# Kernel tuning notes

Hardware: AMD Instinct MI355X
Metric: run time of the kernel (lower is better)

## Reference

```python
import jax, jax.numpy as jnp
import numpy as np

N = 8192       # nodes
F_IN = 512     # input features
H = 8          # heads (layer 1)
C1 = 8         # per-head channels (layer 1)
NC = 16        # num classes
E = 262144     # edges (avg degree 32)
NEG_SLOPE = 0.2


def setup_inputs() -> dict:
    key = jax.random.key(0)
    ks = jax.random.split(key, 11)
    s = 0.1
    return {
        "x": jax.random.normal(ks[0], (N, F_IN), jnp.float32),
        "edge_index": jax.random.randint(ks[1], (2, E), 0, N, dtype=jnp.int32),
        "W1": jax.random.normal(ks[2], (F_IN, H * C1), jnp.float32) * s,
        "a_src1": jax.random.normal(ks[3], (H, C1), jnp.float32) * s,
        "a_dst1": jax.random.normal(ks[4], (H, C1), jnp.float32) * s,
        "b1": jnp.zeros((H * C1,), jnp.float32),
        "W2": jax.random.normal(ks[5], (H * C1, NC), jnp.float32) * s,
        "a_src2": jax.random.normal(ks[6], (1, NC), jnp.float32) * s,
        "a_dst2": jax.random.normal(ks[7], (1, NC), jnp.float32) * s,
        "b2": jnp.zeros((NC,), jnp.float32),
    }


def _gat_layer(x, W, a_src, a_dst, b, src, dst, heads, outc, concat):
    n = x.shape[0]
    h = (x @ W).reshape(n, heads, outc)                      # [N,H,C]
    al_s = jnp.einsum('nhc,hc->nh', h, a_src)                 # [N,H]
    al_d = jnp.einsum('nhc,hc->nh', h, a_dst)                 # [N,H]
    e = jax.nn.leaky_relu(al_s[src] + al_d[dst], NEG_SLOPE)   # [E,H]
    # segment softmax over destination node (every node has a self-loop)
    m = jax.ops.segment_max(e, dst, num_segments=n)
    ex = jnp.exp(e - m[dst])
    denom = jax.ops.segment_sum(ex, dst, num_segments=n)
    alpha = ex / denom[dst]                                   # [E,H]
    out = jax.ops.segment_sum(alpha[:, :, None] * h[src], dst, num_segments=n)  # [N,H,C]
    out = out.reshape(n, heads * outc) if concat else out.mean(axis=1)
    return out + b


def reference(x, edge_index, W1, a_src1, a_dst1, b1, W2, a_src2, a_dst2, b2):
    # add self-loops (PyG GATConv default)
    loop = jnp.arange(N, dtype=edge_index.dtype)
    src = jnp.concatenate([edge_index[0], loop])
    dst = jnp.concatenate([edge_index[1], loop])
    # dropout layers are identity in eval mode
    h1 = jax.nn.elu(_gat_layer(x, W1, a_src1, a_dst1, b1, src, dst, H, C1, True))
    z = _gat_layer(h1, W2, a_src2, a_dst2, b2, src, dst, 1, NC, False)
    return jax.nn.log_softmax(z, axis=-1), z @ z.T
```

## Files before the change

kernel.cpp:

```cpp
#include <hip/hip_runtime.h>
#include <math.h>

#define N_NODES 8192
#define F_IN 512
#define NH1 8
#define C1 8
#define D1 64
#define NC 16
#define E_EDGES 262144
#define TOT_EDGES (E_EDGES + N_NODES)
#define NEG_SLOPE 0.2f

__global__ __launch_bounds__(256) void gemm1_k(const float* __restrict__ x,
                                               const float* __restrict__ W1,
                                               float* __restrict__ h1pre) {
    __shared__ __align__(16) float As[32 * 68];
    __shared__ __align__(16) float Bs[32 * 68];
    int tid = threadIdx.x;
    int rowBase = blockIdx.x * 64;
    int rm = tid >> 4, rn = tid & 15;
    float acc[4][4] = {};
    for (int k0 = 0; k0 < F_IN; k0 += 32) {
#pragma unroll
        for (int j = 0; j < 8; ++j) {
            int i = tid + 256 * j;
            int r = i >> 5, c = i & 31;
            As[c * 68 + r] = x[(rowBase + r) * F_IN + k0 + c];
        }
#pragma unroll
        for (int j = 0; j < 8; ++j) {
            int i = tid + 256 * j;
            int rr = i >> 6, cc = i & 63;
            Bs[rr * 68 + cc] = W1[(k0 + rr) * D1 + cc];
        }
        __syncthreads();
#pragma unroll
        for (int kk = 0; kk < 32; ++kk) {
            float4 a = *(const float4*)&As[kk * 68 + rm * 4];
            float4 b = *(const float4*)&Bs[kk * 68 + rn * 4];
            float av[4] = {a.x, a.y, a.z, a.w};
            float bv[4] = {b.x, b.y, b.z, b.w};
#pragma unroll
            for (int jj = 0; jj < 4; ++jj)
#pragma unroll
                for (int ll = 0; ll < 4; ++ll)
                    acc[jj][ll] = fmaf(av[jj], bv[ll], acc[jj][ll]);
        }
        __syncthreads();
    }
#pragma unroll
    for (int jj = 0; jj < 4; ++jj) {
        float4 o = {acc[jj][0], acc[jj][1], acc[jj][2], acc[jj][3]};
        *(float4*)&h1pre[(size_t)(rowBase + rm * 4 + jj) * D1 + rn * 4] = o;
    }
}

__global__ void logits1_k(const float* __restrict__ h1pre,
                          const float* __restrict__ a_src1, const float* __restrict__ a_dst1,
                          float* __restrict__ als1, float* __restrict__ ald1) {
    int i = blockIdx.x * blockDim.x + threadIdx.x;
    if (i >= N_NODES * NH1) return;
    int h = i & 7;
    const float* hp = h1pre + (size_t)(i >> 3) * D1 + h * C1;
    float s = 0.f, d = 0.f;
#pragma unroll
    for (int c = 0; c < C1; ++c) {
        float v = hp[c];
        s = fmaf(v, a_src1[h * C1 + c], s);
        d = fmaf(v, a_dst1[h * C1 + c], d);
    }
    als1[i] = s;
    ald1[i] = d;
}

__global__ void hist_k(const int* __restrict__ ei, int* __restrict__ counts) {
    int i = blockIdx.x * blockDim.x + threadIdx.x;
    if (i >= TOT_EDGES) return;
    int dst = (i < E_EDGES) ? ei[E_EDGES + i] : (i - E_EDGES);
    atomicAdd(&counts[dst], 1);
}

__global__ __launch_bounds__(1024) void scan_k(const int* __restrict__ counts,
                                               int* __restrict__ offsets, int* __restrict__ cursor) {
    __shared__ int part[1024];
    int t = threadIdx.x;
    int local[8];
    int s = 0;
#pragma unroll
    for (int j = 0; j < 8; ++j) { local[j] = counts[t * 8 + j]; s += local[j]; }
    part[t] = s;
    __syncthreads();
    for (int d = 1; d < 1024; d <<= 1) {
        int v = (t >= d) ? part[t - d] : 0;
        __syncthreads();
        part[t] += v;
        __syncthreads();
    }
    int run = (t == 0) ? 0 : part[t - 1];
#pragma unroll
    for (int j = 0; j < 8; ++j) {
        offsets[t * 8 + j] = run;
        cursor[t * 8 + j] = run;
        run += local[j];
    }
    if (t == 1023) offsets[8192] = run;
}

__global__ void scatter_k(const int* __restrict__ ei, int* __restrict__ cursor, int* __restrict__ csr) {
    int i = blockIdx.x * blockDim.x + threadIdx.x;
    if (i >= TOT_EDGES) return;
    int src, dst;
    if (i < E_EDGES) { src = ei[i]; dst = ei[E_EDGES + i]; }
    else             { src = i - E_EDGES; dst = src; }
    int pos = atomicAdd(&cursor[dst], 1);
    csr[pos] = src;
}

__global__ __launch_bounds__(64) void agg1_k(const float* __restrict__ h1pre,
                                             const float* __restrict__ als1, const float* __restrict__ ald1,
                                             const int* __restrict__ offsets, const int* __restrict__ csr,
                                             const float* __restrict__ b1, float* __restrict__ out1) {
    int n = blockIdx.x, t = threadIdx.x;
    int beg = offsets[n], end = offsets[n + 1];
    int h = t & 7;
    float aldh = ald1[n * NH1 + h];
    float m = -3.4e38f;
    for (int i = beg + (t >> 3); i < end; i += 8) {
        int s = csr[i];
        float v = als1[s * NH1 + h] + aldh;
        v = v > 0.f ? v : NEG_SLOPE * v;
        m = fmaxf(m, v);
    }
    m = fmaxf(m, __shfl_xor(m, 8));
    m = fmaxf(m, __shfl_xor(m, 16));
    m = fmaxf(m, __shfl_xor(m, 32));
    float den = 0.f;
    for (int i = beg + (t >> 3); i < end; i += 8) {
        int s = csr[i];
        float v = als1[s * NH1 + h] + aldh;
        v = v > 0.f ? v : NEG_SLOPE * v;
        den += expf(v - m);
    }
    den += __shfl_xor(den, 8);
    den += __shfl_xor(den, 16);
    den += __shfl_xor(den, 32);
    int q = t >> 3;
    float mq = __shfl(m, q);
    float dq = __shfl(den, q);
    float aldq = ald1[n * NH1 + q];
    float acc = 0.f;
    for (int i = beg; i < end; ++i) {
        int s = csr[i];
        float v = als1[s * NH1 + q] + aldq;
        v = v > 0.f ? v : NEG_SLOPE * v;
        float w = expf(v - mq);
        acc = fmaf(w, h1pre[(size_t)s * D1 + t], acc);
    }
    float val = acc / dq + b1[t];
    out1[(size_t)n * D1 + t] = val > 0.f ? val : expm1f(val);
}

__global__ __launch_bounds__(256) void gemm2_k(const float* __restrict__ out1,
                                               const float* __restrict__ W2,
                                               float* __restrict__ h2pre) {
    __shared__ float w2s[D1 * NC];
    __shared__ float ot[16 * D1];
    int tid = threadIdx.x;
    int nb = blockIdx.x * 16;
#pragma unroll
    for (int j = 0; j < 4; ++j) {
        w2s[tid + 256 * j] = W2[tid + 256 * j];
        ot[tid + 256 * j] = out1[(size_t)nb * D1 + tid + 256 * j];
    }
    __syncthreads();
    int nl = tid >> 4, c = tid & 15;
    float acc = 0.f;
#pragma unroll
    for (int k = 0; k < D1; ++k) acc = fmaf(ot[nl * D1 + k], w2s[k * NC + c], acc);
    h2pre[(size_t)(nb + nl) * NC + c] = acc;
}

__global__ void logits2_k(const float* __restrict__ h2pre,
                          const float* __restrict__ a_src2, const float* __restrict__ a_dst2,
                          float* __restrict__ als2, float* __restrict__ ald2) {
    int n = blockIdx.x * blockDim.x + threadIdx.x;
    if (n >= N_NODES) return;
    const float* hp = h2pre + (size_t)n * NC;
    float s = 0.f, d = 0.f;
#pragma unroll
    for (int c = 0; c < NC; ++c) {
        float v = hp[c];
        s = fmaf(v, a_src2[c], s);
        d = fmaf(v, a_dst2[c], d);
    }
    als2[n] = s;
    ald2[n] = d;
}

__global__ __launch_bounds__(64) void agg2_k(const float* __restrict__ h2pre,
                                             const float* __restrict__ als2, const float* __restrict__ ald2,
                                             const int* __restrict__ offsets, const int* __restrict__ csr,
                                             const float* __restrict__ b2,
                                             float* __restrict__ z, float* __restrict__ out_ls) {
    int n = blockIdx.x, t = threadIdx.x;
    int beg = offsets[n], end = offsets[n + 1];
    float aldn = ald2[n];
    float m = -3.4e38f;
    for (int i = beg + t; i < end; i += 64) {
        float v = als2[csr[i]] + aldn;
        v = v > 0.f ? v : NEG_SLOPE * v;
        m = fmaxf(m, v);
    }
#pragma unroll
    for (int d = 1; d < 64; d <<= 1) m = fmaxf(m, __shfl_xor(m, d));
    float den = 0.f;
    for (int i = beg + t; i < end; i += 64) {
        float v = als2[csr[i]] + aldn;
        v = v > 0.f ? v : NEG_SLOPE * v;
        den += expf(v - m);
    }
#pragma unroll
    for (int d = 1; d < 64; d <<= 1) den += __shfl_xor(den, d);
    int eg = t >> 4, c = t & 15;
    float acc = 0.f;
    for (int i = beg + eg; i < end; i += 4) {
        int s = csr[i];
        float v = als2[s] + aldn;
        v = v > 0.f ? v : NEG_SLOPE * v;
        acc = fmaf(expf(v - m), h2pre[(size_t)s * NC + c], acc);
    }
    acc += __shfl_xor(acc, 16);
    acc += __shfl_xor(acc, 32);
    float zv = acc / den + b2[c];
    if (t < 16) z[(size_t)n * NC + t] = zv;
    float zm = zv;
#pragma unroll
    for (int d = 1; d < 16; d <<= 1) zm = fmaxf(zm, __shfl_xor(zm, d));
    float se = expf(zv - zm);
#pragma unroll
    for (int d = 1; d < 16; d <<= 1) se += __shfl_xor(se, d);
    if (t < 16) out_ls[(size_t)n * NC + t] = zv - (zm + logf(se));
}

__global__ __launch_bounds__(256) void gram_k(const float* __restrict__ z,
                                              float* __restrict__ out) {
    __shared__ __align__(16) float rz[64 * 16];
    int tid = threadIdx.x;
    int colBase = blockIdx.x * 256;
    int rowBase = blockIdx.y * 64;
    ((float4*)rz)[tid] = ((const float4*)z)[rowBase * 4 + tid];
    int j = colBase + tid;
    float c[16];
#pragma unroll
    for (int k4 = 0; k4 < 4; ++k4) {
        float4 v = ((const float4*)(z + (size_t)j * 16))[k4];
        c[k4 * 4 + 0] = v.x; c[k4 * 4 + 1] = v.y; c[k4 * 4 + 2] = v.z; c[k4 * 4 + 3] = v.w;
    }
    __syncthreads();
#pragma unroll 4
    for (int r = 0; r < 64; ++r) {
        const float* zr = &rz[r * 16];
        float acc = 0.f;
#pragma unroll
        for (int k = 0; k < 16; ++k) acc = fmaf(c[k], zr[k], acc);
        out[(size_t)(rowBase + r) * N_NODES + j] = acc;
    }
}

extern "C" void kernel_launch(void* const* d_in, const int* in_sizes, int n_in,
                              void* d_out, int out_size, void* d_ws, size_t ws_size,
                              hipStream_t stream) {
    (void)in_sizes; (void)n_in; (void)out_size; (void)ws_size;
    const float* x      = (const float*)d_in[0];
    const int*   ei     = (const int*)d_in[1];
    const float* W1     = (const float*)d_in[2];
    const float* a_src1 = (const float*)d_in[3];
    const float* a_dst1 = (const float*)d_in[4];
    const float* b1     = (const float*)d_in[5];
    const float* W2     = (const float*)d_in[6];
    const float* a_src2 = (const float*)d_in[7];
    const float* a_dst2 = (const float*)d_in[8];
    const float* b2     = (const float*)d_in[9];
    float* out = (float*)d_out;

    char* ws = (char*)d_ws;
    float* h1pre  = (float*)(ws + 0);
    float* out1   = (float*)(ws + 2097152);
    float* als1   = (float*)(ws + 4194304);
    float* ald1   = (float*)(ws + 4456448);
    float* h2pre  = (float*)(ws + 4718592);
    float* als2   = (float*)(ws + 5242880);
    float* ald2   = (float*)(ws + 5275648);
    float* zarr   = (float*)(ws + 5308416);
    int*   counts = (int*)  (ws + 5832704);
    int*   offsets= (int*)  (ws + 5865472);
    int*   cursor = (int*)  (ws + 5898496);
    int*   csr    = (int*)  (ws + 5931264);

    hipMemsetAsync(counts, 0, N_NODES * sizeof(int), stream);
    hist_k<<<(TOT_EDGES + 255) / 256, 256, 0, stream>>>(ei, counts);
    scan_k<<<1, 1024, 0, stream>>>(counts, offsets, cursor);
    scatter_k<<<(TOT_EDGES + 255) / 256, 256, 0, stream>>>(ei, cursor, csr);

    gemm1_k<<<N_NODES / 64, 256, 0, stream>>>(x, W1, h1pre);
    logits1_k<<<(N_NODES * NH1 + 255) / 256, 256, 0, stream>>>(h1pre, a_src1, a_dst1, als1, ald1);
    agg1_k<<<N_NODES, 64, 0, stream>>>(h1pre, als1, ald1, offsets, csr, b1, out1);

    gemm2_k<<<N_NODES / 16, 256, 0, stream>>>(out1, W2, h2pre);
    logits2_k<<<N_NODES / 256, 256, 0, stream>>>(h2pre, a_src2, a_dst2, als2, ald2);
    agg2_k<<<N_NODES, 64, 0, stream>>>(h2pre, als2, ald2, offsets, csr, b2, zarr, out);

    gram_k<<<dim3(N_NODES / 256, N_NODES / 64), 256, 0, stream>>>(zarr, out + (size_t)N_NODES * NC);
}
```

Baseline: 405.0 us.

## Fuse logits into GEMMs, cache edge weights in LDS, shuffle-based scan

Computes the layer-1 attention logits in the gemm1 epilogue, with the tile halved to 32 rows for more blocks. The layer-2 GEMM and logits move into the agg1 epilogue, which removes three kernel launches and the out1 round trip through memory. agg1 and agg2 now store source indices and exponentiated edge weights in shared memory for nodes with degree up to 128, so the leaky-relu and exp are not recomputed in each pass. Higher-degree nodes fall back to the old path. The scan is rewritten to use wavefront shuffles instead of a shared-memory Hillis-Steele loop with many barriers.

```diff
diff --git a/kernel.cpp b/kernel.cpp
--- a/kernel.cpp
+++ b/kernel.cpp
@@ -10,22 +10,27 @@
 #define E_EDGES 262144
 #define TOT_EDGES (E_EDGES + N_NODES)
 #define NEG_SLOPE 0.2f
+#define CAP 128
 
 __global__ __launch_bounds__(256) void gemm1_k(const float* __restrict__ x,
                                                const float* __restrict__ W1,
-                                               float* __restrict__ h1pre) {
-    __shared__ __align__(16) float As[32 * 68];
+                                               const float* __restrict__ a_src1,
+                                               const float* __restrict__ a_dst1,
+                                               float* __restrict__ h1pre,
+                                               float* __restrict__ als1,
+                                               float* __restrict__ ald1) {
+    __shared__ __align__(16) float As[32 * 34];
     __shared__ __align__(16) float Bs[32 * 68];
     int tid = threadIdx.x;
-    int rowBase = blockIdx.x * 64;
+    int rowBase = blockIdx.x * 32;
     int rm = tid >> 4, rn = tid & 15;
-    float acc[4][4] = {};
+    float acc[2][4] = {};
     for (int k0 = 0; k0 < F_IN; k0 += 32) {
 #pragma unroll
-        for (int j = 0; j < 8; ++j) {
+        for (int j = 0; j < 4; ++j) {
             int i = tid + 256 * j;
             int r = i >> 5, c = i & 31;
-            As[c * 68 + r] = x[(rowBase + r) * F_IN + k0 + c];
+            As[c * 34 + r] = x[(rowBase + r) * F_IN + k0 + c];
         }
 #pragma unroll
         for (int j = 0; j < 8; ++j) {
@@ -36,41 +41,37 @@
         __syncthreads();
 #pragma unroll
         for (int kk = 0; kk < 32; ++kk) {
-            float4 a = *(const float4*)&As[kk * 68 + rm * 4];
+            float2 a = *(const float2*)&As[kk * 34 + rm * 2];
             float4 b = *(const float4*)&Bs[kk * 68 + rn * 4];
-            float av[4] = {a.x, a.y, a.z, a.w};
+            float av[2] = {a.x, a.y};
             float bv[4] = {b.x, b.y, b.z, b.w};
 #pragma unroll
-            for (int jj = 0; jj < 4; ++jj)
+            for (int jj = 0; jj < 2; ++jj)
 #pragma unroll
                 for (int ll = 0; ll < 4; ++ll)
                     acc[jj][ll] = fmaf(av[jj], bv[ll], acc[jj][ll]);
         }
         __syncthreads();
     }
-#pragma unroll
-    for (int jj = 0; jj < 4; ++jj) {
+    int h = rn >> 1, half = rn & 1;
+#pragma unroll
+    for (int jj = 0; jj < 2; ++jj) {
+        int row = rowBase + rm * 2 + jj;
         float4 o = {acc[jj][0], acc[jj][1], acc[jj][2], acc[jj][3]};
-        *(float4*)&h1pre[(size_t)(rowBase + rm * 4 + jj) * D1 + rn * 4] = o;
-    }
-}
-
-__global__ void logits1_k(const float* __restrict__ h1pre,
-                          const float* __restrict__ a_src1, const float* __restrict__ a_dst1,
-                          float* __restrict__ als1, float* __restrict__ ald1) {
-    int i = blockIdx.x * blockDim.x + threadIdx.x;
-    if (i >= N_NODES * NH1) return;
-    int h = i & 7;
-    const float* hp = h1pre + (size_t)(i >> 3) * D1 + h * C1;
-    float s = 0.f, d = 0.f;
-#pragma unroll
-    for (int c = 0; c < C1; ++c) {
-        float v = hp[c];
-        s = fmaf(v, a_src1[h * C1 + c], s);
-        d = fmaf(v, a_dst1[h * C1 + c], d);
-    }
-    als1[i] = s;
-    ald1[i] = d;
+        *(float4*)&h1pre[(size_t)row * D1 + rn * 4] = o;
+        float ps = 0.f, pd = 0.f;
+#pragma unroll
+        for (int ll = 0; ll < 4; ++ll) {
+            ps = fmaf(acc[jj][ll], a_src1[h * C1 + half * 4 + ll], ps);
+            pd = fmaf(acc[jj][ll], a_dst1[h * C1 + half * 4 + ll], pd);
+        }
+        ps += __shfl_xor(ps, 1);
+        pd += __shfl_xor(pd, 1);
+        if (half == 0) {
+            als1[row * NH1 + h] = ps;
+            ald1[row * NH1 + h] = pd;
+        }
+    }
 }
 
 __global__ void hist_k(const int* __restrict__ ei, int* __restrict__ counts) {
@@ -82,21 +83,34 @@
 
 __global__ __launch_bounds__(1024) void scan_k(const int* __restrict__ counts,
                                                int* __restrict__ offsets, int* __restrict__ cursor) {
-    __shared__ int part[1024];
+    __shared__ int wtot[16];
+    __shared__ int wbase[16];
     int t = threadIdx.x;
+    int lane = t & 63, wid = t >> 6;
     int local[8];
     int s = 0;
 #pragma unroll
     for (int j = 0; j < 8; ++j) { local[j] = counts[t * 8 + j]; s += local[j]; }
-    part[t] = s;
-    __syncthreads();
-    for (int d = 1; d < 1024; d <<= 1) {
-        int v = (t >= d) ? part[t - d] : 0;
-        __syncthreads();
-        part[t] += v;
-        __syncthreads();
-    }
-    int run = (t == 0) ? 0 : part[t - 1];
+    int incl = s;
+#pragma unroll
+    for (int d = 1; d < 64; d <<= 1) {
+        int v = __shfl_up(incl, d);
+        if (lane >= d) incl += v;
+    }
+    if (lane == 63) wtot[wid] = incl;
+    __syncthreads();
+    if (t < 16) {
+        int v = wtot[t];
+        int iv = v;
+#pragma unroll
+        for (int d = 1; d < 16; d <<= 1) {
+            int u = __shfl_up(iv, d);
+            if (t >= d) iv += u;
+        }
+        wbase[t] = iv - v;
+    }
+    __syncthreads();
+    int run = wbase[wid] + incl - s;
 #pragma unroll
     for (int j = 0; j < 8; ++j) {
         offsets[t * 8 + j] = run;
@@ -119,82 +133,115 @@
 __global__ __launch_bounds__(64) void agg1_k(const float* __restrict__ h1pre,
                                              const float* __restrict__ als1, const float* __restrict__ ald1,
                                              const int* __restrict__ offsets, const int* __restrict__ csr,
-                                             const float* __restrict__ b1, float* __restrict__ out1) {
+                                             const float* __restrict__ b1,
+                                             const float* __restrict__ W2,
+                                             const float* __restrict__ a_src2, const float* __restrict__ a_dst2,
+                                             float* __restrict__ h2pre,
+                                             float* __restrict__ als2, float* __restrict__ ald2) {
+    __shared__ int   csr_s[CAP];
+    __shared__ float vbuf[CAP * NH1];
+    __shared__ float vals[64];
     int n = blockIdx.x, t = threadIdx.x;
     int beg = offsets[n], end = offsets[n + 1];
-    int h = t & 7;
-    float aldh = ald1[n * NH1 + h];
-    float m = -3.4e38f;
-    for (int i = beg + (t >> 3); i < end; i += 8) {
-        int s = csr[i];
-        float v = als1[s * NH1 + h] + aldh;
-        v = v > 0.f ? v : NEG_SLOPE * v;
-        m = fmaxf(m, v);
-    }
-    m = fmaxf(m, __shfl_xor(m, 8));
-    m = fmaxf(m, __shfl_xor(m, 16));
-    m = fmaxf(m, __shfl_xor(m, 32));
-    float den = 0.f;
-    for (int i = beg + (t >> 3); i < end; i += 8) {
-        int s = csr[i];
-        float v = als1[s * NH1 + h] + aldh;
-        v = v > 0.f ? v : NEG_SLOPE * v;
-        den += expf(v - m);
-    }
-    den += __shfl_xor(den, 8);
-    den += __shfl_xor(den, 16);
-    den += __shfl_xor(den, 32);
-    int q = t >> 3;
-    float mq = __shfl(m, q);
-    float dq = __shfl(den, q);
-    float aldq = ald1[n * NH1 + q];
-    float acc = 0.f;
-    for (int i = beg; i < end; ++i) {
-        int s = csr[i];
-        float v = als1[s * NH1 + q] + aldq;
-        v = v > 0.f ? v : NEG_SLOPE * v;
-        float w = expf(v - mq);
-        acc = fmaf(w, h1pre[(size_t)s * D1 + t], acc);
-    }
-    float val = acc / dq + b1[t];
-    out1[(size_t)n * D1 + t] = val > 0.f ? val : expm1f(val);
-}
-
-__global__ __launch_bounds__(256) void gemm2_k(const float* __restrict__ out1,
-                                               const float* __restrict__ W2,
-                                               float* __restrict__ h2pre) {
-    __shared__ float w2s[D1 * NC];
-    __shared__ float ot[16 * D1];
-    int tid = threadIdx.x;
-    int nb = blockIdx.x * 16;
-#pragma unroll
-    for (int j = 0; j < 4; ++j) {
-        w2s[tid + 256 * j] = W2[tid + 256 * j];
-        ot[tid + 256 * j] = out1[(size_t)nb * D1 + tid + 256 * j];
-    }
-    __syncthreads();
-    int nl = tid >> 4, c = tid & 15;
-    float acc = 0.f;
-#pragma unroll
-    for (int k = 0; k < D1; ++k) acc = fmaf(ot[nl * D1 + k], w2s[k * NC + c], acc);
-    h2pre[(size_t)(nb + nl) * NC + c] = acc;
-}
-
-__global__ void logits2_k(const float* __restrict__ h2pre,
-                          const float* __restrict__ a_src2, const float* __restrict__ a_dst2,
-                          float* __restrict__ als2, float* __restrict__ ald2) {
-    int n = blockIdx.x * blockDim.x + threadIdx.x;
-    if (n >= N_NODES) return;
-    const float* hp = h2pre + (size_t)n * NC;
-    float s = 0.f, d = 0.f;
-#pragma unroll
-    for (int c = 0; c < NC; ++c) {
-        float v = hp[c];
-        s = fmaf(v, a_src2[c], s);
-        d = fmaf(v, a_dst2[c], d);
-    }
-    als2[n] = s;
-    ald2[n] = d;
+    int deg = end - beg;
+    float val;
+    if (deg <= CAP) {
+        int h = t & 7, eo = t >> 3;
+        float aldh = ald1[n * NH1 + h];
+        float m = -3.4e38f;
+        for (int e = eo; e < deg; e += 8) {
+            int s = csr[beg + e];
+            if (h == 0) csr_s[e] = s;
+            float v = als1[s * NH1 + h] + aldh;
+            v = v > 0.f ? v : NEG_SLOPE * v;
+            vbuf[e * NH1 + h] = v;
+            m = fmaxf(m, v);
+        }
+        m = fmaxf(m, __shfl_xor(m, 8));
+        m = fmaxf(m, __shfl_xor(m, 16));
+        m = fmaxf(m, __shfl_xor(m, 32));
+        float den = 0.f;
+        for (int e = eo; e < deg; e += 8) {
+            float w = expf(vbuf[e * NH1 + h] - m);
+            vbuf[e * NH1 + h] = w;
+            den += w;
+        }
+        den += __shfl_xor(den, 8);
+        den += __shfl_xor(den, 16);
+        den += __shfl_xor(den, 32);
+        __syncthreads();
+        int q = t >> 3;
+        float dq = __shfl(den, q);
+        float acc = 0.f;
+        int e = 0;
+        for (; e + 4 <= deg; e += 4) {
+            int s0 = csr_s[e], s1 = csr_s[e + 1], s2 = csr_s[e + 2], s3 = csr_s[e + 3];
+            float w0 = vbuf[e * NH1 + q], w1 = vbuf[(e + 1) * NH1 + q];
+            float w2 = vbuf[(e + 2) * NH1 + q], w3 = vbuf[(e + 3) * NH1 + q];
+            acc = fmaf(w0, h1pre[s0 * D1 + t], acc);
+            acc = fmaf(w1, h1pre[s1 * D1 + t], acc);
+            acc = fmaf(w2, h1pre[s2 * D1 + t], acc);
+            acc = fmaf(w3, h1pre[s3 * D1 + t], acc);
+        }
+        for (; e < deg; ++e)
+            acc = fmaf(vbuf[e * NH1 + q], h1pre[csr_s[e] * D1 + t], acc);
+        val = acc / dq + b1[t];
+    } else {
+        int h = t & 7;
+        float aldh = ald1[n * NH1 + h];
+        float m = -3.4e38f;
+        for (int i = beg + (t >> 3); i < end; i += 8) {
+            int s = csr[i];
+            float v = als1[s * NH1 + h] + aldh;
+            v = v > 0.f ? v : NEG_SLOPE * v;
+            m = fmaxf(m, v);
+        }
+        m = fmaxf(m, __shfl_xor(m, 8));
+        m = fmaxf(m, __shfl_xor(m, 16));
+        m = fmaxf(m, __shfl_xor(m, 32));
+        float den = 0.f;
+        for (int i = beg + (t >> 3); i < end; i += 8) {
+            int s = csr[i];
+            float v = als1[s * NH1 + h] + aldh;
+            v = v > 0.f ? v : NEG_SLOPE * v;
+            den += expf(v - m);
+        }
+        den += __shfl_xor(den, 8);
+        den += __shfl_xor(den, 16);
+        den += __shfl_xor(den, 32);
+        int q = t >> 3;
+        float mq = __shfl(m, q);
+        float dq = __shfl(den, q);
+        float aldq = ald1[n * NH1 + q];
+        float acc = 0.f;
+        for (int i = beg; i < end; ++i) {
+            int s = csr[i];
+            float v = als1[s * NH1 + q] + aldq;
+            v = v > 0.f ? v : NEG_SLOPE * v;
+            acc = fmaf(expf(v - mq), h1pre[s * D1 + t], acc);
+        }
+        val = acc / dq + b1[t];
+    }
+    val = val > 0.f ? val : expm1f(val);
+    __syncthreads();
+    vals[t] = val;
+    __syncthreads();
+    int g = t >> 4, c = t & 15;
+    float a2 = 0.f;
+    const float* w2p = W2 + g * 16 * NC + c;
+#pragma unroll
+    for (int j = 0; j < 16; ++j)
+        a2 = fmaf(vals[g * 16 + j], w2p[j * NC], a2);
+    a2 += __shfl_xor(a2, 16);
+    a2 += __shfl_xor(a2, 32);
+    if (t < 16) h2pre[(size_t)n * NC + t] = a2;
+    float ps = a2 * a_src2[c], pd = a2 * a_dst2[c];
+#pragma unroll
+    for (int d = 1; d < 16; d <<= 1) {
+        ps += __shfl_xor(ps, d);
+        pd += __shfl_xor(pd, d);
+    }
+    if (t == 0) { als2[n] = ps; ald2[n] = pd; }
 }
 
 __global__ __launch_bounds__(64) void agg2_k(const float* __restrict__ h2pre,
@@ -202,36 +249,76 @@
                                              const int* __restrict__ offsets, const int* __restrict__ csr,
                                              const float* __restrict__ b2,
                                              float* __restrict__ z, float* __restrict__ out_ls) {
+    __shared__ int   csr2[CAP];
+    __shared__ float wb2[CAP];
     int n = blockIdx.x, t = threadIdx.x;
     int beg = offsets[n], end = offsets[n + 1];
+    int deg = end - beg;
     float aldn = ald2[n];
-    float m = -3.4e38f;
-    for (int i = beg + t; i < end; i += 64) {
-        float v = als2[csr[i]] + aldn;
-        v = v > 0.f ? v : NEG_SLOPE * v;
-        m = fmaxf(m, v);
-    }
-#pragma unroll
-    for (int d = 1; d < 64; d <<= 1) m = fmaxf(m, __shfl_xor(m, d));
-    float den = 0.f;
-    for (int i = beg + t; i < end; i += 64) {
-        float v = als2[csr[i]] + aldn;
-        v = v > 0.f ? v : NEG_SLOPE * v;
-        den += expf(v - m);
-    }
-#pragma unroll
-    for (int d = 1; d < 64; d <<= 1) den += __shfl_xor(den, d);
     int eg = t >> 4, c = t & 15;
-    float acc = 0.f;
-    for (int i = beg + eg; i < end; i += 4) {
-        int s = csr[i];
-        float v = als2[s] + aldn;
-        v = v > 0.f ? v : NEG_SLOPE * v;
-        acc = fmaf(expf(v - m), h2pre[(size_t)s * NC + c], acc);
-    }
-    acc += __shfl_xor(acc, 16);
-    acc += __shfl_xor(acc, 32);
-    float zv = acc / den + b2[c];
+    float zv;
+    if (deg <= CAP) {
+        float m = -3.4e38f;
+        for (int i = t; i < deg; i += 64) {
+            int s = csr[beg + i];
+            csr2[i] = s;
+            float v = als2[s] + aldn;
+            v = v > 0.f ? v : NEG_SLOPE * v;
+            wb2[i] = v;
+            m = fmaxf(m, v);
+        }
+#pragma unroll
+        for (int d = 1; d < 64; d <<= 1) m = fmaxf(m, __shfl_xor(m, d));
+        float den = 0.f;
+        for (int i = t; i < deg; i += 64) {
+            float w = expf(wb2[i] - m);
+            wb2[i] = w;
+            den += w;
+        }
+#pragma unroll
+        for (int d = 1; d < 64; d <<= 1) den += __shfl_xor(den, d);
+        __syncthreads();
+        float acc = 0.f;
+        int e = eg;
+        for (; e + 4 < deg; e += 8) {
+            int s0 = csr2[e], s1 = csr2[e + 4];
+            float w0 = wb2[e], w1 = wb2[e + 4];
+            acc = fmaf(w0, h2pre[s0 * NC + c], acc);
+            acc = fmaf(w1, h2pre[s1 * NC + c], acc);
+        }
+        for (; e < deg; e += 4)
+            acc = fmaf(wb2[e], h2pre[csr2[e] * NC + c], acc);
+        acc += __shfl_xor(acc, 16);
+        acc += __shfl_xor(acc, 32);
+        zv = acc / den + b2[c];
+    } else {
+        float m = -3.4e38f;
+        for (int i = beg + t; i < end; i += 64) {
+            float v = als2[csr[i]] + aldn;
+            v = v > 0.f ? v : NEG_SLOPE * v;
+            m = fmaxf(m, v);
+        }
+#pragma unroll
+        for (int d = 1; d < 64; d <<= 1) m = fmaxf(m, __shfl_xor(m, d));
+        float den = 0.f;
+        for (int i = beg + t; i < end; i += 64) {
+            float v = als2[csr[i]] + aldn;
+            v = v > 0.f ? v : NEG_SLOPE * v;
+            den += expf(v - m);
+        }
+#pragma unroll
+        for (int d = 1; d < 64; d <<= 1) den += __shfl_xor(den, d);
+        float acc = 0.f;
+        for (int i = beg + eg; i < end; i += 4) {
+            int s = csr[i];
+            float v = als2[s] + aldn;
+            v = v > 0.f ? v : NEG_SLOPE * v;
+            acc = fmaf(expf(v - m), h2pre[(size_t)s * NC + c], acc);
+        }
+        acc += __shfl_xor(acc, 16);
+        acc += __shfl_xor(acc, 32);
+        zv = acc / den + b2[c];
+    }
     if (t < 16) z[(size_t)n * NC + t] = zv;
     float zm = zv;
 #pragma unroll
@@ -285,7 +372,6 @@
 
     char* ws = (char*)d_ws;
     float* h1pre  = (float*)(ws + 0);
-    float* out1   = (float*)(ws + 2097152);
     float* als1   = (float*)(ws + 4194304);
     float* ald1   = (float*)(ws + 4456448);
     float* h2pre  = (float*)(ws + 4718592);
@@ -302,12 +388,9 @@
     scan_k<<<1, 1024, 0, stream>>>(counts, offsets, cursor);
     scatter_k<<<(TOT_EDGES + 255) / 256, 256, 0, stream>>>(ei, cursor, csr);
 
-    gemm1_k<<<N_NODES / 64, 256, 0, stream>>>(x, W1, h1pre);
-    logits1_k<<<(N_NODES * NH1 + 255) / 256, 256, 0, stream>>>(h1pre, a_src1, a_dst1, als1, ald1);
-    agg1_k<<<N_NODES, 64, 0, stream>>>(h1pre, als1, ald1, offsets, csr, b1, out1);
-
-    gemm2_k<<<N_NODES / 16, 256, 0, stream>>>(out1, W2, h2pre);
-    logits2_k<<<N_NODES / 256, 256, 0, stream>>>(h2pre, a_src2, a_dst2, als2, ald2);
+    gemm1_k<<<N_NODES / 32, 256, 0, stream>>>(x, W1, a_src1, a_dst1, h1pre, als1, ald1);
+    agg1_k<<<N_NODES, 64, 0, stream>>>(h1pre, als1, ald1, offsets, csr, b1,
+                                       W2, a_src2, a_dst2, h2pre, als2, ald2);
     agg2_k<<<N_NODES, 64, 0, stream>>>(h2pre, als2, ald2, offsets, csr, b2, zarr, out);
 
     gram_k<<<dim3(N_NODES / 256, N_NODES / 64), 256, 0, stream>>>(zarr, out + (size_t)N_NODES * NC);
```

New measurement: 368.3 us. -9.1%, faster.
